# Kernel tuning notes

Hardware: AMD Instinct MI355X
Metric: run time of the kernel (lower is better)

## Reference

```python
import jax, jax.numpy as jnp
import numpy as np

# Module hyperparameters
P_, K_, NH = 8, 4, 8
B, H, W, C = 2, 64, 24, 256


def setup_inputs() -> dict:
    key = jax.random.key(0)
    ks = jax.random.split(key, 16)

    def w(k, shape, s=0.02):
        return (jax.random.normal(k, shape) * s).astype(jnp.float32)

    z = lambda *shape: jnp.zeros(shape, jnp.float32)
    return {
        'x_2d': jax.random.normal(ks[0], (B, H, W, C), dtype=jnp.float32),
        # block projections (used as x @ W + b)
        'wq_proj': w(ks[1], (C, C)), 'bq_proj': z(C),
        'wk_proj': w(ks[2], (C, C)), 'bk_proj': z(C),
        'wv_proj': w(ks[3], (C, C)), 'bv_proj': z(C),
        # routing attention projections
        'wq_a': w(ks[4], (C, C)), 'bq_a': z(C),
        'wk_a': w(ks[5], (C, C)), 'bk_a': z(C),
        'wv_a': w(ks[6], (C, C)), 'bv_a': z(C),
        'wo_a': w(ks[7], (C, C)), 'bo_a': z(C),
        # global conv path (HWIO, 5x5, SAME padding == torch padding=2)
        'conv_w': w(ks[8], (5, 5, C, C)), 'conv_b': z(C),
        # layer norms
        'ln1_g': jnp.ones((C,), jnp.float32), 'ln1_b': z(C),
        'ln2_g': jnp.ones((C,), jnp.float32), 'ln2_b': z(C),
    }


def _layer_norm(t, g, b, eps=1e-5):
    m = t.mean(-1, keepdims=True)
    v = ((t - m) ** 2).mean(-1, keepdims=True)
    return (t - m) / jnp.sqrt(v + eps) * g + b


def reference(x_2d, wq_proj, bq_proj, wk_proj, bk_proj, wv_proj, bv_proj,
              wq_a, bq_a, wk_a, bk_a, wv_a, bv_a, wo_a, bo_a,
              conv_w, conv_b, ln1_g, ln1_b, ln2_g, ln2_b):
    Bb, Hh, Ww, Cc = x_2d.shape
    hp = Hh // P_                      # block height
    dk = Cc // NH
    kv = min(K_, P_)

    x_p = x_2d.reshape(Bb, P_, hp, Ww, Cc)
    q_p = x_p @ wq_proj + bq_proj
    k_p = x_p @ wk_proj + bk_proj
    v_p = x_p @ wv_proj + bv_proj

    # block-level routing: mean-pooled block descriptors -> top-k blocks
    q_loc = q_p.mean((2, 3))           # [B,P,C]
    k_loc = k_p.mean((2, 3))
    S_loc = jnp.einsum('bpc,bqc->bpq', q_loc, k_loc)
    _, R = jax.lax.top_k(S_loc, kv)    # [B,P,kv] int32 indices into P

    # gather routed K/V blocks: [B,P,kv,hp*W,C]
    k_flat = k_p.reshape(Bb, P_, hp * Ww, Cc)
    v_flat = v_p.reshape(Bb, P_, hp * Ww, Cc)
    k_fil = jax.vmap(lambda t, r: t[r])(k_flat, R).reshape(Bb, P_, kv, hp, Ww, Cc)
    v_fil = jax.vmap(lambda t, r: t[r])(v_flat, R).reshape(Bb, P_, kv, hp, Ww, Cc)
    q_un = jnp.broadcast_to(q_p[:, :, None], (Bb, P_, kv, hp, Ww, Cc))

    # multi-head attention over flattened (kv*hp*W) per block p
    L = kv * hp * Ww
    def to_heads(t, w, b):
        t = t @ w + b
        t = t.reshape(Bb, P_, kv, hp, Ww, NH, dk)
        return t.transpose(0, 5, 1, 2, 3, 4, 6).reshape(Bb, NH, P_, L, dk)

    qh = to_heads(q_un, wq_a, bq_a)
    kh = to_heads(k_fil, wk_a, bk_a)
    vh = to_heads(v_fil, wv_a, bv_a)

    scores = jnp.einsum('bhpqd,bhpkd->bhpqk', qh, kh) / jnp.sqrt(jnp.float32(dk))
    attn = jax.nn.softmax(scores, axis=-1)
    ctx = jnp.einsum('bhpqk,bhpkd->bhpqd', attn, vh)
    # 'b h p (k hp w) dk -> b p k hp w (h dk)'
    ctx = ctx.reshape(Bb, NH, P_, kv, hp, Ww, dk).transpose(0, 2, 3, 4, 5, 1, 6)
    ctx = ctx.reshape(Bb, P_, kv, hp, Ww, Cc)
    routing_out = (ctx @ wo_a + bo_a).mean(2)          # [B,P,hp,W,C]

    x_res = _layer_norm(x_p + routing_out, ln1_g, ln1_b)

    # global conv path (NHWC SAME conv, kernel 5)
    kv_g = (k_p + v_p).reshape(Bb, Hh, Ww, Cc)
    g = jax.lax.conv_general_dilated(kv_g, conv_w, (1, 1), 'SAME',
                                     dimension_numbers=('NHWC', 'HWIO', 'NHWC')) + conv_b
    g = g.reshape(Bb, P_, hp, Ww, Cc)

    out = _layer_norm(x_res + g, ln2_g, ln2_b)
    return out.reshape(Bb, Hh, Ww, Cc)
```

## Files before the change

### kernel.cpp

```cpp
#include <hip/hip_runtime.h>
#include <hip/hip_bf16.h>


#define NPOS 3072
#define CD   256
#define NE   (NPOS*CD)

typedef short bf16x8 __attribute__((ext_vector_type(8)));
typedef float f32x4  __attribute__((ext_vector_type(4)));

__device__ inline ushort f2bf(float f) {
    __hip_bfloat16 h = __float2bfloat16(f);
    return *reinterpret_cast<ushort*>(&h);
}
__device__ inline float bf2f(ushort u) {
    unsigned v = ((unsigned)u) << 16;
    return *reinterpret_cast<float*>(&v);
}
__device__ inline bf16x8 addbf(bf16x8 a, bf16x8 b) {
    bf16x8 o;
    #pragma unroll
    for (int j = 0; j < 8; ++j)
        o[j] = (short)f2bf(bf2f((ushort)a[j]) + bf2f((ushort)b[j]));
    return o;
}

__global__ __launch_bounds__(256) void wtransA(
    const float* __restrict__ w0, const float* __restrict__ w1, const float* __restrict__ w2,
    const float* __restrict__ w3, const float* __restrict__ w4, const float* __restrict__ w5,
    const float* __restrict__ w6, const float* __restrict__ cw,
    ushort* __restrict__ wt, ushort* __restrict__ wct, ushort* __restrict__ wstr,
    const float* __restrict__ x,
    const float* __restrict__ bq, const float* __restrict__ bk,
    float* __restrict__ qloc, float* __restrict__ kloc)
{
    __shared__ float l[64*65];
    int blk = blockIdx.x;
    int tid = threadIdx.x;
    if (blk < 512) {
        const float* M;
        ushort* D;
        int r2;
        if (blk < 112) {
            int mat = blk >> 4; r2 = blk & 15;
            M = mat==0?w0:mat==1?w1:mat==2?w2:mat==3?w3:mat==4?w4:mat==5?w5:w6;
            D = wt + (size_t)mat*65536;
        } else {
            int b2 = blk - 112;
            int tap = b2 >> 4; r2 = b2 & 15;
            M = cw + (size_t)tap*65536;
            D = wct + (size_t)tap*65536;
        }
        int ci0 = (r2 >> 2)*64, co0 = (r2 & 3)*64;
        int a = tid >> 6, c = tid & 63;
        #pragma unroll 4
        for (int k = 0; k < 16; ++k) {
            int cil = k*4 + a;
            l[cil*65 + c] = M[(size_t)(ci0 + cil)*256 + co0 + c];
        }
        __syncthreads();
        #pragma unroll 4
        for (int k = 0; k < 16; ++k) {
            int col = k*4 + a;
            D[((size_t)(co0 + col))*256 + ci0 + c] = f2bf(l[c*65 + col]);
        }
    } else if (blk < 524) {
        int b2 = blk - 512;
        int mat = b2 >> 2, quarter = b2 & 3;
        const float* M = mat==0 ? w0 : (mat==1 ? w1 : w2);
        size_t base = (size_t)quarter*16384;
        #pragma unroll
        for (int i = 0; i < 16; ++i) {
            size_t idx = base + (size_t)i*1024 + tid*4;
            float4 v = *(const float4*)(M + idx);
            ushort4 o;
            o.x = f2bf(v.x); o.y = f2bf(v.y); o.z = f2bf(v.z); o.w = f2bf(v.w);
            *(ushort4*)(wstr + (size_t)mat*65536 + idx) = o;
        }
    } else {
        int q2 = blk - 524;
        int bp = q2 & 15, which = q2 >> 4;
        int c = tid;
        float s = 0.f;
        for (int i = 0; i < 192; ++i)
            s += x[((size_t)(bp*192 + i))*256 + c];
        l[c] = s * (1.0f/192.0f);
        __syncthreads();
        const float* W  = which ? w1 : w0;
        const float* Bv = which ? bk : bq;
        float* dst      = which ? kloc : qloc;
        float acc = Bv[c];
        #pragma unroll 8
        for (int k = 0; k < 256; ++k)
            acc += l[k] * W[(size_t)k*256 + c];
        dst[bp*256 + c] = acc;
    }
}

__global__ __launch_bounds__(256) void compose(
    const ushort* __restrict__ wt7, const ushort* __restrict__ wstr,
    const float* __restrict__ bq, const float* __restrict__ bk, const float* __restrict__ bv,
    const float* __restrict__ bqa, const float* __restrict__ bka, const float* __restrict__ bva,
    ushort* __restrict__ wtc, ushort* __restrict__ wtkv, float* __restrict__ bcomp)
{
    int y = blockIdx.y;
    int tid = threadIdx.x;
    if (y < 3) {
        __shared__ __align__(16) ushort As[32*264];
        const ushort* A = wt7 + (size_t)(3 + y)*65536;
        const ushort* T = wstr + (size_t)y*65536;
        ushort* U = wtc + (size_t)y*65536;
        int m0 = (blockIdx.x >> 1)*32;
        int nh = blockIdx.x & 1;
        #pragma unroll
        for (int i = 0; i < 4; ++i) {
            int c = i*256 + tid;
            int pos = c >> 5, off = (c & 31)*8;
            *(bf16x8*)&As[pos*264 + off] = *(const bf16x8*)(A + (size_t)(m0 + pos)*256 + off);
        }
        __syncthreads();
        int w = tid >> 6, lane = tid & 63, lm = lane & 15, lq = lane >> 4;
        const ushort* tb = T + ((size_t)(nh*128 + w*32 + lm))*256 + lq*8;
        f32x4 acc[2][2];
        #pragma unroll
        for (int mt = 0; mt < 2; ++mt)
            #pragma unroll
            for (int nt = 0; nt < 2; ++nt) acc[mt][nt] = (f32x4){0.f,0.f,0.f,0.f};
        for (int kc = 0; kc < 8; ++kc) {
            bf16x8 bw[2];
            #pragma unroll
            for (int nt = 0; nt < 2; ++nt) bw[nt] = *(const bf16x8*)(tb + nt*4096 + kc*32);
            bf16x8 af[2];
            #pragma unroll
            for (int mt = 0; mt < 2; ++mt)
                af[mt] = *(const bf16x8*)&As[(mt*16 + lm)*264 + kc*32 + lq*8];
            #pragma unroll
            for (int mt = 0; mt < 2; ++mt)
                #pragma unroll
                for (int nt = 0; nt < 2; ++nt)
                    acc[mt][nt] = __builtin_amdgcn_mfma_f32_16x16x32_bf16(af[mt], bw[nt], acc[mt][nt], 0,0,0);
        }
        #pragma unroll
        for (int mt = 0; mt < 2; ++mt)
            #pragma unroll
            for (int nt = 0; nt < 2; ++nt) {
                int n = nh*128 + w*32 + nt*16 + lm;
                #pragma unroll
                for (int j = 0; j < 4; ++j) {
                    int m = m0 + mt*16 + lq*4 + j;
                    U[(size_t)m*256 + n] = f2bf(acc[mt][nt][j]);
                }
            }
    } else {
        const ushort* wk7 = wt7 + 65536;
        const ushort* wv7 = wt7 + 131072;
        size_t base = (size_t)blockIdx.x*4096 + tid*16;
        #pragma unroll
        for (int i = 0; i < 2; ++i) {
            bf16x8 a = *(const bf16x8*)(wk7 + base + i*8);
            bf16x8 b = *(const bf16x8*)(wv7 + base + i*8);
            *(bf16x8*)(wtkv + base + i*8) = addbf(a, b);
        }
        int bx = blockIdx.x;
        if (bx < 3) {
            const float* bsrc = bx==0 ? bq : (bx==1 ? bk : bv);
            const float* basr = bx==0 ? bqa : (bx==1 ? bka : bva);
            const ushort* wa = wt7 + (size_t)(3 + bx)*65536;
            float s = basr[tid];
            for (int k = 0; k < 256; ++k)
                s += bsrc[k] * bf2f(wa[(size_t)tid*256 + k]);
            bcomp[bx*256 + tid] = s;
        } else if (bx == 3) {
            bcomp[3*256 + tid] = bk[tid] + bv[tid];
        }
    }
}

__global__ void topk_kern(const float* __restrict__ qloc, const float* __restrict__ kloc,
                          int* __restrict__ Rix)
{
    __shared__ float S[64];
    int b = blockIdx.x, t = threadIdx.x;
    int p = t >> 3, qq = t & 7;
    float s = 0.f;
    for (int c = 0; c < 256; ++c)
        s += qloc[(b*8+p)*256 + c] * kloc[(b*8+qq)*256 + c];
    S[t] = s;
    __syncthreads();
    if (t < 8) {
        float vals[8];
        #pragma unroll
        for (int j = 0; j < 8; ++j) vals[j] = S[t*8 + j];
        for (int j = 0; j < 4; ++j) {
            int best = 0; float bv = vals[0];
            #pragma unroll
            for (int i = 1; i < 8; ++i) if (vals[i] > bv) { bv = vals[i]; best = i; }
            Rix[(b*8 + t)*4 + j] = best;
            vals[best] = -1e30f;
        }
    }
}

__global__ __launch_bounds__(256) void gemm_quad(
    const float* __restrict__ A,
    const ushort* __restrict__ wtc, const ushort* __restrict__ wtkv,
    const float* __restrict__ bcomp,
    ushort* __restrict__ U0, ushort* __restrict__ U1,
    ushort* __restrict__ U2, ushort* __restrict__ U3)
{
    __shared__ __align__(16) ushort As[32*264];
    int y = blockIdx.y;
    const ushort* T = (y < 3) ? (wtc + (size_t)y*65536) : wtkv;
    const float* Bi = bcomp + y*256;
    ushort* U = y==0 ? U0 : (y==1 ? U1 : (y==2 ? U2 : U3));
    float sc = (y == 0) ? 0.17677669529663687f : 1.0f;
    int tid = threadIdx.x;
    int m0 = (blockIdx.x >> 1)*32;
    int nh = blockIdx.x & 1;
    #pragma unroll
    for (int i = 0; i < 4; ++i) {
        int c = i*256 + tid;
        int pos = c >> 5, off = (c & 31)*8;
        const float* src = A + (size_t)(m0 + pos)*256 + off;
        float4 v0 = *(const float4*)src;
        float4 v1 = *(const float4*)(src + 4);
        ushort4 o0, o1;
        o0.x = f2bf(v0.x); o0.y = f2bf(v0.y); o0.z = f2bf(v0.z); o0.w = f2bf(v0.w);
        o1.x = f2bf(v1.x); o1.y = f2bf(v1.y); o1.z = f2bf(v1.z); o1.w = f2bf(v1.w);
        *(ushort4*)&As[pos*264 + off]     = o0;
        *(ushort4*)&As[pos*264 + off + 4] = o1;
    }
    __syncthreads();
    int w = tid >> 6, lane = tid & 63, lm = lane & 15, lq = lane >> 4;
    const ushort* tb = T + ((size_t)(nh*128 + w*32 + lm))*256 + lq*8;

    f32x4 acc[2][2];
    #pragma unroll
    for (int mt = 0; mt < 2; ++mt)
        #pragma unroll
        for (int nt = 0; nt < 2; ++nt) acc[mt][nt] = (f32x4){0.f,0.f,0.f,0.f};

    bf16x8 bw[2];
    #pragma unroll
    for (int nt = 0; nt < 2; ++nt) bw[nt] = *(const bf16x8*)(tb + nt*4096);

    for (int kc = 0; kc < 8; ++kc) {
        int nk = (kc + 1 < 8) ? kc + 1 : 7;
        bf16x8 bn[2];
        #pragma unroll
        for (int nt = 0; nt < 2; ++nt) bn[nt] = *(const bf16x8*)(tb + nt*4096 + nk*32);
        bf16x8 af[2];
        #pragma unroll
        for (int mt = 0; mt < 2; ++mt)
            af[mt] = *(const bf16x8*)&As[(mt*16 + lm)*264 + kc*32 + lq*8];
        #pragma unroll
        for (int mt = 0; mt < 2; ++mt)
            #pragma unroll
            for (int nt = 0; nt < 2; ++nt)
                acc[mt][nt] = __builtin_amdgcn_mfma_f32_16x16x32_bf16(af[mt], bw[nt], acc[mt][nt], 0,0,0);
        #pragma unroll
        for (int nt = 0; nt < 2; ++nt) bw[nt] = bn[nt];
    }

    #pragma unroll
    for (int mt = 0; mt < 2; ++mt) {
        #pragma unroll
        for (int nt = 0; nt < 2; ++nt) {
            int n = nh*128 + w*32 + nt*16 + lm;
            float bb = Bi[n];
            #pragma unroll
            for (int j = 0; j < 4; ++j) {
                int m = m0 + mt*16 + lq*4 + j;
                U[(size_t)m*256 + n] = f2bf((acc[mt][nt][j] + bb) * sc);
            }
        }
    }
}

__global__ __launch_bounds__(256) void attn_conv(
    const ushort* __restrict__ qab, const ushort* __restrict__ kab,
    const ushort* __restrict__ vab, const int* __restrict__ Rix,
    float* __restrict__ pl, ushort* __restrict__ pacc,
    const ushort* __restrict__ kvc,
    const ushort* __restrict__ wct, ushort* __restrict__ pconv)
{
    __shared__ __align__(16) ushort SMEM[19008];
    int tid = threadIdx.x;
    int bid = blockIdx.x;
    if (bid < 640) {
        int ch = bid & 1;
        int t2 = bid >> 1;
        int rp = t2 / 5, dy = t2 - rp*5;
        int b = rp >> 5, y0 = (rp & 31)*2;

        const bf16x8 zero8 = (bf16x8){0,0,0,0,0,0,0,0};
        #pragma unroll
        for (int i = 0; i < 7; ++i) {
            int c = i*256 + tid;
            int row = (c >= 896);
            int cc = c - row*896;
            int pos = cc >> 5, off = (cc & 31)*8;
            int y = y0 + row + dy - 2;
            bf16x8 v = zero8;
            if (y >= 0 && y < 64 && pos >= 2 && pos < 26) {
                size_t sb = ((size_t)((b*64 + y)*24 + (pos - 2)))*256 + off;
                v = *(const bf16x8*)(kvc + sb);
            }
            *(bf16x8*)(&SMEM[row*9504 + pos*264 + off]) = v;
        }
        __syncthreads();

        int w = tid >> 6;
        int lane = tid & 63, lm = lane & 15, lq = lane >> 4;
        const ushort* bbase = wct + ((size_t)((dy*5)*256 + ch*128 + w*32 + lm))*256 + lq*8;
        const ushort* a00 = &SMEM[lm*264 + lq*8];

        f32x4 acc[2][2][2];
        #pragma unroll
        for (int r = 0; r < 2; ++r)
            #pragma unroll
            for (int mt = 0; mt < 2; ++mt)
                #pragma unroll
                for (int nt = 0; nt < 2; ++nt)
                    acc[r][mt][nt] = (f32x4){0.f,0.f,0.f,0.f};

        bf16x8 b0[2], b1[2];
        #pragma unroll
        for (int nt = 0; nt < 2; ++nt) b0[nt] = *(const bf16x8*)(bbase + nt*4096);
        #pragma unroll
        for (int nt = 0; nt < 2; ++nt) b1[nt] = *(const bf16x8*)(bbase + 32 + nt*4096);

        for (int iter = 0; iter < 40; ++iter) {
            int i2 = (iter + 2 < 40) ? iter + 2 : 39;
            int boff = (i2 >> 3)*65536 + (i2 & 7)*32;
            bf16x8 bn[2];
            #pragma unroll
            for (int nt = 0; nt < 2; ++nt) bn[nt] = *(const bf16x8*)(bbase + boff + nt*4096);

            int aoff = (iter >> 3)*264 + (iter & 7)*32;
            bf16x8 af[2][2];
            #pragma unroll
            for (int r = 0; r < 2; ++r)
                #pragma unroll
                for (int mt = 0; mt < 2; ++mt)
                    af[r][mt] = *(const bf16x8*)(a00 + r*9504 + mt*4224 + aoff);

            #pragma unroll
            for (int r = 0; r < 2; ++r)
                #pragma unroll
                for (int mt = 0; mt < 2; ++mt)
                    #pragma unroll
                    for (int nt = 0; nt < 2; ++nt)
                        acc[r][mt][nt] = __builtin_amdgcn_mfma_f32_16x16x32_bf16(
                            af[r][mt], b0[nt], acc[r][mt][nt], 0, 0, 0);

            #pragma unroll
            for (int nt = 0; nt < 2; ++nt) { b0[nt] = b1[nt]; b1[nt] = bn[nt]; }
        }

        #pragma unroll
        for (int r = 0; r < 2; ++r) {
            int grow = rp*2 + r;
            #pragma unroll
            for (int mt = 0; mt < 2; ++mt) {
                #pragma unroll
                for (int nt = 0; nt < 2; ++nt) {
                    int cob = ch*128 + w*32 + nt*16 + lm;
                    #pragma unroll
                    for (int j = 0; j < 4; ++j) {
                        int x = mt*16 + lq*4 + j;
                        if (x < 24)
                            pconv[((size_t)(dy*3072 + grow*24 + x))*256 + cob]
                                = f2bf(acc[r][mt][nt][j]);
                    }
                }
            }
        }
    } else {
        int id = bid - 640;
        int bph = id >> 2, kvb = id & 3;
        int w = tid >> 6, lane = tid & 63;
        int lm = lane & 15, lq = lane >> 4;
        int bp = bph >> 3, h = bph & 7, b = bp >> 3;
        int r = Rix[bp*4 + kvb];
        int vrow0 = (b*8 + r)*192;
        ushort* P  = SMEM;
        ushort* Vs = SMEM + 2560;

        #pragma unroll
        for (int i = 0; i < 6; ++i) {
            int idx = i*256 + tid;
            int pos = idx >> 3, c4 = (idx & 7)*4;
            ushort4 v = *(const ushort4*)(vab + ((size_t)(vrow0 + pos))*256 + h*32 + c4);
            Vs[(c4+0)*200 + pos] = v.x;
            Vs[(c4+1)*200 + pos] = v.y;
            Vs[(c4+2)*200 + pos] = v.z;
            Vs[(c4+3)*200 + pos] = v.w;
        }

        bf16x8 qf[3];
        #pragma unroll
        for (int t = 0; t < 3; ++t)
            qf[t] = *(const bf16x8*)(qab + ((size_t)(bp*192 + w*48 + t*16 + lm))*256 + h*32 + lq*8);

        const ushort* kbase = kab + ((size_t)(vrow0))*256 + h*32 + lq*8;
        ushort* pw = P + w*640;
        __syncthreads();

        f32x4 O[3][2];
        #pragma unroll
        for (int t = 0; t < 3; ++t) { O[t][0] = (f32x4){0,0,0,0}; O[t][1] = (f32x4){0,0,0,0}; }
        float l[3] = {0.f, 0.f, 0.f};

        for (int k0 = 0; k0 < 192; k0 += 32) {
            bf16x8 kf0 = *(const bf16x8*)(kbase + (size_t)(k0 + lm)*256);
            bf16x8 kf1 = *(const bf16x8*)(kbase + (size_t)(k0 + 16 + lm)*256);
            bf16x8 vf0 = *(const bf16x8*)(&Vs[lm*200 + k0 + lq*8]);
            bf16x8 vf1 = *(const bf16x8*)(&Vs[(16 + lm)*200 + k0 + lq*8]);
            #pragma unroll
            for (int t = 0; t < 3; ++t) {
                f32x4 s0 = __builtin_amdgcn_mfma_f32_16x16x32_bf16(kf0, qf[t], (f32x4){0,0,0,0}, 0,0,0);
                f32x4 s1 = __builtin_amdgcn_mfma_f32_16x16x32_bf16(kf1, qf[t], (f32x4){0,0,0,0}, 0,0,0);
                float p0[4], p1[4];
                #pragma unroll
                for (int j = 0; j < 4; ++j) { p0[j] = __expf(s0[j]); p1[j] = __expf(s1[j]); }
                l[t] += p0[0]+p0[1]+p0[2]+p0[3] + p1[0]+p1[1]+p1[2]+p1[3];
                ushort4 a, c;
                a.x = f2bf(p0[0]); a.y = f2bf(p0[1]); a.z = f2bf(p0[2]); a.w = f2bf(p0[3]);
                c.x = f2bf(p1[0]); c.y = f2bf(p1[1]); c.z = f2bf(p1[2]); c.w = f2bf(p1[3]);
                *(ushort4*)(pw + lm*40 + lq*4)      = a;
                *(ushort4*)(pw + lm*40 + 16 + lq*4) = c;
                bf16x8 pf = *(const bf16x8*)(pw + lm*40 + lq*8);
                O[t][0] = __builtin_amdgcn_mfma_f32_16x16x32_bf16(pf, vf0, O[t][0], 0,0,0);
                O[t][1] = __builtin_amdgcn_mfma_f32_16x16x32_bf16(pf, vf1, O[t][1], 0,0,0);
            }
        }

        #pragma unroll
        for (int t = 0; t < 3; ++t) {
            float lt = l[t];
            lt += __shfl_xor(lt, 16);
            lt += __shfl_xor(lt, 32);
            size_t pbase = ((size_t)(bph*4 + kvb))*192 + w*48 + t*16;
            if (lq == 0) pl[pbase + lm] = lt;
            #pragma unroll
            for (int nt = 0; nt < 2; ++nt)
                #pragma unroll
                for (int reg = 0; reg < 4; ++reg)
                    pacc[(pbase + lq*4 + reg)*32 + nt*16 + lm] = f2bf(O[t][nt][reg]);
        }
    }
}

__global__ __launch_bounds__(256) void gemm_wo_ln2(
    const float* __restrict__ pl, const ushort* __restrict__ pacc,
    const ushort* __restrict__ T, const float* __restrict__ boa,
    const float* __restrict__ x,
    const float* __restrict__ g1, const float* __restrict__ b1,
    const ushort* __restrict__ pc, const float* __restrict__ cb,
    const float* __restrict__ g2, const float* __restrict__ b2,
    float* __restrict__ out)
{
    __shared__ __align__(16) ushort As[32*264];
    __shared__ float L2x[32*256];
    int tid = threadIdx.x;
    int m0 = blockIdx.x*32;
    #pragma unroll
    for (int i = 0; i < 4; ++i) {
        int c = i*256 + tid;
        int pos = c >> 5, off = (c & 31)*8;
        int m = m0 + pos;
        int bp = m / 192, q = m - bp*192;
        int h = off >> 5, d0 = off & 31;
        int bph = bp*8 + h;
        float ls = 0.f;
        float cv[8] = {0,0,0,0,0,0,0,0};
        #pragma unroll
        for (int k = 0; k < 4; ++k) {
            size_t pidx = ((size_t)(bph*4 + k))*192 + q;
            ls += pl[pidx];
            bf16x8 pv = *(const bf16x8*)(pacc + pidx*32 + d0);
            #pragma unroll
            for (int j = 0; j < 8; ++j) cv[j] += bf2f((ushort)pv[j]);
        }
        ushort o[8];
        #pragma unroll
        for (int j = 0; j < 8; ++j) o[j] = f2bf(cv[j] / ls);
        *(ushort4*)&As[pos*264 + off]     = make_ushort4(o[0],o[1],o[2],o[3]);
        *(ushort4*)&As[pos*264 + off + 4] = make_ushort4(o[4],o[5],o[6],o[7]);
    }
    __syncthreads();
    int w = tid >> 6, lane = tid & 63, lm = lane & 15, lq = lane >> 4;
    const ushort* tb = T + ((size_t)(w*64 + lm))*256 + lq*8;

    f32x4 acc[2][4];
    #pragma unroll
    for (int mt = 0; mt < 2; ++mt)
        #pragma unroll
        for (int nt = 0; nt < 4; ++nt) acc[mt][nt] = (f32x4){0.f,0.f,0.f,0.f};

    bf16x8 bw[4];
    #pragma unroll
    for (int nt = 0; nt < 4; ++nt) bw[nt] = *(const bf16x8*)(tb + nt*4096);

    for (int kc = 0; kc < 8; ++kc) {
        int nk = (kc + 1 < 8) ? kc + 1 : 7;
        bf16x8 bn[4];
        #pragma unroll
        for (int nt = 0; nt < 4; ++nt) bn[nt] = *(const bf16x8*)(tb + nt*4096 + nk*32);
        bf16x8 af[2];
        #pragma unroll
        for (int mt = 0; mt < 2; ++mt)
            af[mt] = *(const bf16x8*)&As[(mt*16 + lm)*264 + kc*32 + lq*8];
        #pragma unroll
        for (int mt = 0; mt < 2; ++mt)
            #pragma unroll
            for (int nt = 0; nt < 4; ++nt)
                acc[mt][nt] = __builtin_amdgcn_mfma_f32_16x16x32_bf16(af[mt], bw[nt], acc[mt][nt], 0,0,0);
        #pragma unroll
        for (int nt = 0; nt < 4; ++nt) bw[nt] = bn[nt];
    }

    #pragma unroll
    for (int mt = 0; mt < 2; ++mt) {
        #pragma unroll
        for (int nt = 0; nt < 4; ++nt) {
            int n = w*64 + nt*16 + lm;
            float bb = boa[n];
            #pragma unroll
            for (int j = 0; j < 4; ++j) {
                int pos = mt*16 + lq*4 + j;
                float val = acc[mt][nt][j] + bb;
                L2x[pos*256 + n] = val + x[(size_t)(m0 + pos)*256 + n];
            }
        }
    }
    __syncthreads();
    #pragma unroll
    for (int rr = 0; rr < 8; ++rr) {
        int pos = w*8 + rr;
        int grow = m0 + pos;
        float4 a = *(const float4*)(&L2x[pos*256 + lane*4]);
        float x0 = a.x, x1 = a.y, x2 = a.z, x3 = a.w;
        float s  = x0 + x1 + x2 + x3;
        float sq = x0*x0 + x1*x1 + x2*x2 + x3*x3;
        #pragma unroll
        for (int off = 32; off > 0; off >>= 1) {
            s  += __shfl_xor(s,  off);
            sq += __shfl_xor(sq, off);
        }
        float mean = s * (1.0f/256.0f);
        float var  = sq * (1.0f/256.0f) - mean*mean;
        float rstd = rsqrtf(var + 1e-5f);
        float4 gv = *(const float4*)(g1 + lane*4);
        float4 bv = *(const float4*)(b1 + lane*4);
        float r0 = (x0 - mean)*rstd*gv.x + bv.x;
        float r1 = (x1 - mean)*rstd*gv.y + bv.y;
        float r2 = (x2 - mean)*rstd*gv.z + bv.z;
        float r3 = (x3 - mean)*rstd*gv.w + bv.w;
        size_t base = (size_t)grow*256 + lane*4;
        float4 gsum = *(const float4*)(cb + lane*4);
        #pragma unroll
        for (int d = 0; d < 5; ++d) {
            ushort4 v = *(const ushort4*)(pc + (size_t)d*NE + base);
            gsum.x += bf2f(v.x); gsum.y += bf2f(v.y);
            gsum.z += bf2f(v.z); gsum.w += bf2f(v.w);
        }
        float y0 = r0 + gsum.x, y1 = r1 + gsum.y, y2 = r2 + gsum.z, y3 = r3 + gsum.w;
        float s2v  = y0 + y1 + y2 + y3;
        float sq2  = y0*y0 + y1*y1 + y2*y2 + y3*y3;
        #pragma unroll
        for (int off = 32; off > 0; off >>= 1) {
            s2v += __shfl_xor(s2v, off);
            sq2 += __shfl_xor(sq2, off);
        }
        float mean2 = s2v * (1.0f/256.0f);
        float var2  = sq2 * (1.0f/256.0f) - mean2*mean2;
        float rstd2 = rsqrtf(var2 + 1e-5f);
        float4 g2v = *(const float4*)(g2 + lane*4);
        float4 b2v = *(const float4*)(b2 + lane*4);
        float4 o;
        o.x = (y0 - mean2)*rstd2*g2v.x + b2v.x;
        o.y = (y1 - mean2)*rstd2*g2v.y + b2v.y;
        o.z = (y2 - mean2)*rstd2*g2v.z + b2v.z;
        o.w = (y3 - mean2)*rstd2*g2v.w + b2v.w;
        *(float4*)(out + base) = o;
    }
}

extern "C" void kernel_launch(void* const* d_in, const int* in_sizes, int n_in,
                              void* d_out, int out_size, void* d_ws, size_t ws_size,
                              hipStream_t stream)
{
    (void)in_sizes; (void)n_in; (void)out_size; (void)ws_size;
    const float* x    = (const float*)d_in[0];
    const float* wq   = (const float*)d_in[1];
    const float* bq   = (const float*)d_in[2];
    const float* wk   = (const float*)d_in[3];
    const float* bk   = (const float*)d_in[4];
    const float* wv   = (const float*)d_in[5];
    const float* bv   = (const float*)d_in[6];
    const float* wqa  = (const float*)d_in[7];
    const float* bqa  = (const float*)d_in[8];
    const float* wka  = (const float*)d_in[9];
    const float* bka  = (const float*)d_in[10];
    const float* wva  = (const float*)d_in[11];
    const float* bva  = (const float*)d_in[12];
    const float* woa  = (const float*)d_in[13];
    const float* boa  = (const float*)d_in[14];
    const float* cw   = (const float*)d_in[15];
    const float* cbi  = (const float*)d_in[16];
    const float* ln1g = (const float*)d_in[17];
    const float* ln1b = (const float*)d_in[18];
    const float* ln2g = (const float*)d_in[19];
    const float* ln2b = (const float*)d_in[20];
    float* out = (float*)d_out;

    float* ws = (float*)d_ws;
    const size_t HNE = NE/2;
    ushort* qab = (ushort*)(ws + 0*HNE);
    ushort* kab = (ushort*)(ws + 1*HNE);
    ushort* vab = (ushort*)(ws + 2*HNE);
    ushort* kvc = (ushort*)(ws + 3*HNE);
    float* R    = ws + 4*HNE;
    ushort* pacc = (ushort*)R;
    float*  pl   = R + 1572864;
    ushort* pconv= (ushort*)(R + 1671168);
    ushort* wt7  = (ushort*)(R + 3637248);
    ushort* wstr = wt7 + 458752;
    ushort* wtc  = wstr + 196608;
    ushort* wtkv = wtc + 196608;
    ushort* wct  = wtkv + 65536;
    float* bcomp = (float*)(wct + 1638400);
    float* qloc  = bcomp + 1024;
    float* kloc  = qloc + 4096;
    int*   Rix   = (int*)(kloc + 4096);

    wtransA<<<556, 256, 0, stream>>>(wq,wk,wv,wqa,wka,wva,woa, cw, wt7, wct, wstr,
                                     x, bq, bk, qloc, kloc);
    compose<<<dim3(16,4), 256, 0, stream>>>(wt7, wstr, bq,bk,bv, bqa,bka,bva,
                                            wtc, wtkv, bcomp);
    topk_kern<<<2, 64, 0, stream>>>(qloc, kloc, Rix);
    gemm_quad<<<dim3(192,4), 256, 0, stream>>>(x, wtc, wtkv, bcomp, qab, kab, vab, kvc);
    attn_conv<<<1152, 256, 0, stream>>>(qab, kab, vab, Rix, pl, pacc, kvc, wct, pconv);
    gemm_wo_ln2<<<96, 256, 0, stream>>>(pl, pacc, wt7 + 393216, boa, x, ln1g, ln1b,
                                        pconv, cbi, ln2g, ln2b, out);
}
```

Measured before the change: 199.9 us.

## Fuse topk into compose kernel and interleave conv/attention block scheduling

Moves the top-k routing computation into an extra grid row of the compose kernel, removing a separate tiny kernel launch. Remaps attn_conv block indices so conv and attention blocks are interleaved in groups of nine instead of all conv blocks first, aiming at better load balance across CUs. The shared buffer is hoisted to kernel scope so the topk path can reuse it; extra idle blocks in the new grid row exit immediately.

Result: faster. 192.1 us (-3.9%).

```diff
diff --git a/kernel.cpp b/kernel.cpp
--- a/kernel.cpp
+++ b/kernel.cpp
@@ -101,12 +101,13 @@
     const ushort* __restrict__ wt7, const ushort* __restrict__ wstr,
     const float* __restrict__ bq, const float* __restrict__ bk, const float* __restrict__ bv,
     const float* __restrict__ bqa, const float* __restrict__ bka, const float* __restrict__ bva,
-    ushort* __restrict__ wtc, ushort* __restrict__ wtkv, float* __restrict__ bcomp)
+    ushort* __restrict__ wtc, ushort* __restrict__ wtkv, float* __restrict__ bcomp,
+    const float* __restrict__ qloc, const float* __restrict__ kloc, int* __restrict__ Rix)
 {
+    __shared__ __align__(16) ushort As[32*264];
     int y = blockIdx.y;
     int tid = threadIdx.x;
     if (y < 3) {
-        __shared__ __align__(16) ushort As[32*264];
         const ushort* A = wt7 + (size_t)(3 + y)*65536;
         const ushort* T = wstr + (size_t)y*65536;
         ushort* U = wtc + (size_t)y*65536;
@@ -151,7 +152,7 @@
                     U[(size_t)m*256 + n] = f2bf(acc[mt][nt][j]);
                 }
             }
-    } else {
+    } else if (y == 3) {
         const ushort* wk7 = wt7 + 65536;
         const ushort* wv7 = wt7 + 131072;
         size_t base = (size_t)blockIdx.x*4096 + tid*16;
@@ -173,30 +174,29 @@
         } else if (bx == 3) {
             bcomp[3*256 + tid] = bk[tid] + bv[tid];
         }
-    }
-}
-
-__global__ void topk_kern(const float* __restrict__ qloc, const float* __restrict__ kloc,
-                          int* __restrict__ Rix)
-{
-    __shared__ float S[64];
-    int b = blockIdx.x, t = threadIdx.x;
-    int p = t >> 3, qq = t & 7;
-    float s = 0.f;
-    for (int c = 0; c < 256; ++c)
-        s += qloc[(b*8+p)*256 + c] * kloc[(b*8+qq)*256 + c];
-    S[t] = s;
-    __syncthreads();
-    if (t < 8) {
-        float vals[8];
-        #pragma unroll
-        for (int j = 0; j < 8; ++j) vals[j] = S[t*8 + j];
-        for (int j = 0; j < 4; ++j) {
-            int best = 0; float bv = vals[0];
-            #pragma unroll
-            for (int i = 1; i < 8; ++i) if (vals[i] > bv) { bv = vals[i]; best = i; }
-            Rix[(b*8 + t)*4 + j] = best;
-            vals[best] = -1e30f;
+    } else {
+        if (blockIdx.x >= 2) return;
+        float* S = (float*)As;
+        int b = blockIdx.x, t = tid;
+        if (t < 64) {
+            int p = t >> 3, qq = t & 7;
+            float s = 0.f;
+            for (int c = 0; c < 256; ++c)
+                s += qloc[(b*8+p)*256 + c] * kloc[(b*8+qq)*256 + c];
+            S[t] = s;
+        }
+        __syncthreads();
+        if (t < 8) {
+            float vals[8];
+            #pragma unroll
+            for (int j = 0; j < 8; ++j) vals[j] = S[t*8 + j];
+            for (int j = 0; j < 4; ++j) {
+                int best = 0; float bv2 = vals[0];
+                #pragma unroll
+                for (int i = 1; i < 8; ++i) if (vals[i] > bv2) { bv2 = vals[i]; best = i; }
+                Rix[(b*8 + t)*4 + j] = best;
+                vals[best] = -1e30f;
+            }
         }
     }
 }
@@ -286,10 +286,11 @@
 {
     __shared__ __align__(16) ushort SMEM[19008];
     int tid = threadIdx.x;
-    int bid = blockIdx.x;
-    if (bid < 640) {
-        int ch = bid & 1;
-        int t2 = bid >> 1;
+    int grp = blockIdx.x / 9, rem = blockIdx.x - grp*9;
+    if (rem < 5) {
+        int cid = grp*5 + rem;
+        int ch = cid & 1;
+        int t2 = cid >> 1;
         int rp = t2 / 5, dy = t2 - rp*5;
         int b = rp >> 5, y0 = (rp & 31)*2;
 
@@ -377,8 +378,8 @@
             }
         }
     } else {
-        int id = bid - 640;
-        int bph = id >> 2, kvb = id & 3;
+        int aid = grp*4 + (rem - 5);
+        int bph = aid >> 2, kvb = aid & 3;
         int w = tid >> 6, lane = tid & 63;
         int lm = lane & 15, lq = lane >> 4;
         int bp = bph >> 3, h = bph & 7, b = bp >> 3;
@@ -638,9 +639,8 @@
 
     wtransA<<<556, 256, 0, stream>>>(wq,wk,wv,wqa,wka,wva,woa, cw, wt7, wct, wstr,
                                      x, bq, bk, qloc, kloc);
-    compose<<<dim3(16,4), 256, 0, stream>>>(wt7, wstr, bq,bk,bv, bqa,bka,bva,
-                                            wtc, wtkv, bcomp);
-    topk_kern<<<2, 64, 0, stream>>>(qloc, kloc, Rix);
+    compose<<<dim3(16,5), 256, 0, stream>>>(wt7, wstr, bq,bk,bv, bqa,bka,bva,
+                                            wtc, wtkv, bcomp, qloc, kloc, Rix);
     gemm_quad<<<dim3(192,4), 256, 0, stream>>>(x, wtc, wtkv, bcomp, qab, kab, vab, kvc);
     attn_conv<<<1152, 256, 0, stream>>>(qab, kab, vab, Rix, pl, pacc, kvc, wct, pconv);
     gemm_wo_ln2<<<96, 256, 0, stream>>>(pl, pacc, wt7 + 393216, boa, x, ln1g, ln1b,
```
